# Kernel optimization log

Hardware: AMD Instinct MI355X
Metric: run time of the kernel (lower is better)

## Reference

```python
import jax, jax.numpy as jnp
import numpy as np

B = 128          # episodes
L = 512          # static pad length per episode (support or query)
LAMBDA_K_TAU = 0.1


def _masked_cov(x, mask, lengths):
    # x: [B, L, D]; mask: [B, L, 1]; lengths: [B] (float counts)
    x = x * mask
    mean = x.sum(axis=1) / lengths[:, None]                    # [B, D]
    c = (x - mean[:, None, :]) * mask                          # [B, L, D]
    cov = jnp.einsum('bld,ble->bde', c, c)                     # [B, D, D]
    return cov / (lengths - 1.0)[:, None, None]


def _calc_label_cov_inv(task_cov, label_cov):
    d = task_cov.shape[-1]
    eye = jnp.eye(d, dtype=task_cov.dtype)
    m = LAMBDA_K_TAU * label_cov + (1.0 - LAMBDA_K_TAU) * task_cov + 0.1 * eye
    return jnp.linalg.inv(m)


def _separate_qsl(graph_reprs, labels, is_query, batch_index):
    # Re-batch flat [N, D] into padded per-episode support/query tensors.
    N, D = graph_reprs.shape
    g = batch_index * 2 + is_query                             # group id
    perm = jnp.argsort(g)                                      # stable sort
    gs = g[perm]
    first = jnp.searchsorted(gs, gs, side='left')
    rank = jnp.arange(N) - first                               # index within group
    b = batch_index[perm]
    q = is_query[perm]
    row_s = jnp.where(q == 0, rank, L)                         # dummy row L for other kind
    row_q = jnp.where(q == 1, rank, L)
    xp = graph_reprs[perm]
    sup = jnp.zeros((B, L + 1, D), graph_reprs.dtype).at[b, row_s].set(xp)[:, :L]
    qry = jnp.zeros((B, L + 1, D), graph_reprs.dtype).at[b, row_q].set(xp)[:, :L]
    sup_lab = jnp.zeros((B, L + 1), labels.dtype).at[b, row_s].set(labels[perm])[:, :L]
    isq = is_query.astype(jnp.float32)
    sup_len = jnp.zeros((B,), jnp.float32).at[batch_index].add(1.0 - isq)
    qry_len = jnp.zeros((B,), jnp.float32).at[batch_index].add(isq)
    return sup, sup_lab, sup_len, qry, qry_len


def setup_inputs() -> dict:
    key = jax.random.key(0)
    k0, k1, k2, k3 = jax.random.split(key, 4)
    N, D = 49152, 512
    graph_reprs = jax.random.normal(k0, (N, D), jnp.float32)
    labels = jax.random.randint(k1, (N,), 0, 2)
    is_query = jax.random.randint(k2, (N,), 0, 2)
    batch_index = jnp.sort(jax.random.randint(k3, (N,), 0, B))
    log_scale = jnp.full((1,), np.log(1.0 / 16.0), jnp.float32)
    return {"graph_reprs": graph_reprs, "log_scale": log_scale,
            "labels": labels, "is_query": is_query, "batch_index": batch_index}


def reference(graph_reprs, log_scale, labels, is_query, batch_index):
    sup, sup_lab, sup_len, qry, qry_len = _separate_qsl(graph_reprs, labels, is_query, batch_index)
    f = jnp.float32
    support_mask = (jnp.arange(L)[None, :] < sup_len[:, None]).astype(f)[..., None]  # [B,L,1]
    mpos = (sup_lab == 1).astype(f)[..., None] * support_mask
    mneg = (sup_lab == 0).astype(f)[..., None] * support_mask

    pos_mean = (sup * mpos).sum(axis=1) / mpos.sum(axis=1)     # [B, D]
    neg_mean = (sup * mneg).sum(axis=1) / mneg.sum(axis=1)

    task_cov = _masked_cov(sup, support_mask, sup_len)
    pos_cnt = mpos.sum(axis=(1, 2))
    neg_cnt = mneg.sum(axis=(1, 2))
    # Masked covariance == cov of boolean-extracted, re-batched class subsets.
    pos_cov = _masked_cov(sup, mpos, pos_cnt)
    neg_cov = _masked_cov(sup, mneg, neg_cnt)

    pos_inv = _calc_label_cov_inv(task_cov, pos_cov)
    neg_inv = _calc_label_cov_inv(task_cov, neg_cov)

    query_mask = (jnp.arange(L)[None, :] < qry_len[:, None]).astype(f)  # [B, L]
    pos_diff = qry - pos_mean[:, None, :]
    neg_diff = qry - neg_mean[:, None, :]
    # Faithful to original einsum (sums inv over its second index):
    pos_maha = jnp.einsum('bik,bkx,bij->bi', pos_diff, pos_inv, pos_diff) * query_mask
    neg_maha = jnp.einsum('bik,bkx,bij->bi', neg_diff, neg_inv, neg_diff) * query_mask

    logits = jnp.stack([neg_maha, pos_maha], axis=-1)          # [B, L, 2]
    return logits * jnp.exp(log_scale)
```

## Files before the change

### kernel.cpp

```cpp
#include <hip/hip_runtime.h>
#include <cstdint>
#include <cstddef>

#define EPISODES 128
#define LPAD     512
#define DDIM     512
#define NS_CAP   320
#define GTILE    64
#define NPAIRS   15
#define CG_ITERS 14
#define GL_F4    9984
#define KCH      64
#define XBF_ROW  1024

typedef __attribute__((ext_vector_type(8))) __bf16 bf16x8;
typedef __attribute__((ext_vector_type(4))) float  floatx4;

__device__ __forceinline__ int lower_bound_dev(const int* __restrict__ a, int n, int key){
    int lo = 0, hi = n;
    while(lo < hi){
        int m = (lo + hi) >> 1;
        if(a[m] < key) lo = m + 1; else hi = m;
    }
    return lo;
}

__device__ __forceinline__ float4 f4add(float4 a, float4 b){
    return make_float4(a.x+b.x, a.y+b.y, a.z+b.z, a.w+b.w);
}
__device__ __forceinline__ float4 f4fma(float s, float4 a, float4 acc){
    return make_float4(acc.x + s*a.x, acc.y + s*a.y, acc.z + s*a.z, acc.w + s*a.w);
}
__device__ __forceinline__ float f4dot(float4 a, float4 b){
    return a.x*b.x + a.y*b.y + a.z*b.z + a.w*b.w;
}
__device__ __forceinline__ float f4sum(float4 a){ return (a.x+a.y)+(a.z+a.w); }

__device__ __forceinline__ unsigned short f2bf(float x){
    unsigned u = __float_as_uint(x);
    u += 0x7FFFu + ((u >> 16) & 1u);
    return (unsigned short)(u >> 16);
}
__device__ __forceinline__ float bf2f(unsigned short h){
    return __uint_as_float(((unsigned)h) << 16);
}
__device__ __forceinline__ void cvt_hilo(float4 x, ushort4& hh, ushort4& ll){
    hh.x = f2bf(x.x); ll.x = f2bf(x.x - bf2f(hh.x));
    hh.y = f2bf(x.y); ll.y = f2bf(x.y - bf2f(hh.y));
    hh.z = f2bf(x.z); ll.z = f2bf(x.z - bf2f(hh.z));
    hh.w = f2bf(x.w); ll.w = f2bf(x.w - bf2f(hh.w));
}

__device__ __forceinline__ float rdlanef(float v, int l){
    return __int_as_float(__builtin_amdgcn_readlane(__float_as_int(v), l));
}
__device__ __forceinline__ float dotb(float4 g, float4 u, int l){
    return g.x*rdlanef(u.x,l) + g.y*rdlanef(u.y,l)
         + g.z*rdlanef(u.z,l) + g.w*rdlanef(u.w,l);
}
__device__ __forceinline__ void gload_lds16(const void* g, void* l){
    __builtin_amdgcn_global_load_lds(
        (const __attribute__((address_space(1))) void*)g,
        (__attribute__((address_space(3))) void*)l,
        16, 0, 0);
}

__global__ __launch_bounds__(256) void k_prep(
        const int* __restrict__ labels, const int* __restrict__ is_query,
        const int* __restrict__ bidx, const float* __restrict__ X, int N,
        int* __restrict__ sup_idx, int* __restrict__ qry_idx,
        int* __restrict__ sup_lab, int* __restrict__ counts,
        float* __restrict__ task_mean, float* __restrict__ pos_mean,
        float* __restrict__ neg_mean, float* __restrict__ row_sums2,
        unsigned short* __restrict__ Xbf)
{
    const int bid  = blockIdx.x;
    const int b    = bid >> 1;
    const int h    = bid & 1;
    const int tid  = threadIdx.x;
    const int lane = tid & 63;
    const int wave = tid >> 6;

    __shared__ int s_start, s_end;
    __shared__ int wq[4];
    __shared__ int s_runq, s_npos;
    __shared__ int   sidx[NS_CAP];
    __shared__ float slabf[NS_CAP];
    __shared__ float4 pa[4][64];
    __shared__ float4 pp[4][64];

    if(tid == 0){
        s_start = lower_bound_dev(bidx, N, b);
        s_end   = lower_bound_dev(bidx, N, b + 1);
        s_runq  = 0;
        s_npos  = 0;
    }
    __syncthreads();
    const int start = s_start, end = s_end;

    for(int base = start; base < end; base += 256){
        int idx   = base + tid;
        bool valid = idx < end;
        int q   = valid ? is_query[idx] : 0;
        int lab = valid ? labels[idx]   : 0;
        unsigned long long m = __ballot(q == 1);
        if(lane == 0) wq[wave] = __popcll(m);
        __syncthreads();
        int woff = 0;
        for(int w = 0; w < wave; w++) woff += wq[w];
        int qbefore = __popcll(m & ((1ull << lane) - 1ull)) + woff;
        int runq0 = s_runq;
        int chunk_total = wq[0] + wq[1] + wq[2] + wq[3];
        if(valid){
            int pos_in_seg = idx - start;
            if(q){
                int qr = runq0 + qbefore;
                if(h == 0 && qr < LPAD) qry_idx[b * LPAD + qr] = idx;
            } else {
                int sr = pos_in_seg - runq0 - qbefore;
                if(sr < LPAD){
                    if(h == 0){
                        sup_idx[b * LPAD + sr] = idx;
                        sup_lab[b * LPAD + sr] = lab;
                    }
                    if(sr < NS_CAP){ sidx[sr] = idx; slabf[sr] = (float)lab; }
                    if(lab == 1) atomicAdd(&s_npos, 1);
                }
            }
        }
        __syncthreads();
        if(tid == 0) s_runq = runq0 + chunk_total;
        __syncthreads();
    }

    const int nq   = s_runq;
    const int ns   = (end - start) - nq;
    const int npos = s_npos;
    const int nneg = ns - npos;
    if(h == 0 && tid == 0){
        counts[b*4 + 0] = ns;
        counts[b*4 + 1] = nq;
        counts[b*4 + 2] = npos;
        counts[b*4 + 3] = nneg;
    }
    const int nsb = min(ns, NS_CAP);

    const float4* X4 = (const float4*)X;
    const int colg = h*64 + lane;
    float4 sa = make_float4(0.f,0.f,0.f,0.f);
    float4 sp = make_float4(0.f,0.f,0.f,0.f);
    int r = wave;
    for(; r + 12 < nsb; r += 16){
        int n0 = sidx[r], n1 = sidx[r+4], n2 = sidx[r+8], n3 = sidx[r+12];
        float l0 = slabf[r], l1 = slabf[r+4], l2 = slabf[r+8], l3 = slabf[r+12];
        float4 x0 = X4[(size_t)n0*128 + colg];
        float4 x1 = X4[(size_t)n1*128 + colg];
        float4 x2 = X4[(size_t)n2*128 + colg];
        float4 x3 = X4[(size_t)n3*128 + colg];
        sa = f4add(sa, f4add(f4add(x0,x1), f4add(x2,x3)));
        sp = f4fma(l0,x0, f4fma(l1,x1, f4fma(l2,x2, f4fma(l3,x3, sp))));
        {
            ushort4 hh, ll;
            size_t rb;
            rb = ((size_t)(b*NS_CAP + r   ) << 10);
            cvt_hilo(x0, hh, ll);
            *(ushort4*)&Xbf[rb + colg*4] = hh;  *(ushort4*)&Xbf[rb + 512 + colg*4] = ll;
            rb = ((size_t)(b*NS_CAP + r+4 ) << 10);
            cvt_hilo(x1, hh, ll);
            *(ushort4*)&Xbf[rb + colg*4] = hh;  *(ushort4*)&Xbf[rb + 512 + colg*4] = ll;
            rb = ((size_t)(b*NS_CAP + r+8 ) << 10);
            cvt_hilo(x2, hh, ll);
            *(ushort4*)&Xbf[rb + colg*4] = hh;  *(ushort4*)&Xbf[rb + 512 + colg*4] = ll;
            rb = ((size_t)(b*NS_CAP + r+12) << 10);
            cvt_hilo(x3, hh, ll);
            *(ushort4*)&Xbf[rb + colg*4] = hh;  *(ushort4*)&Xbf[rb + 512 + colg*4] = ll;
        }
        float r0s = f4sum(x0), r1s = f4sum(x1), r2s = f4sum(x2), r3s = f4sum(x3);
        #pragma unroll
        for(int off = 32; off; off >>= 1){
            r0s += __shfl_xor(r0s, off); r1s += __shfl_xor(r1s, off);
            r2s += __shfl_xor(r2s, off); r3s += __shfl_xor(r3s, off);
        }
        if(lane == 0){
            row_sums2[(b*LPAD + r   )*2 + h] = r0s;
            row_sums2[(b*LPAD + r+4 )*2 + h] = r1s;
            row_sums2[(b*LPAD + r+8 )*2 + h] = r2s;
            row_sums2[(b*LPAD + r+12)*2 + h] = r3s;
        }
    }
    for(; r < nsb; r += 4){
        int n = sidx[r];
        float l = slabf[r];
        float4 x = X4[(size_t)n*128 + colg];
        sa = f4add(sa, x);
        sp = f4fma(l, x, sp);
        {
            ushort4 hh, ll;
            size_t rb = ((size_t)(b*NS_CAP + r) << 10);
            cvt_hilo(x, hh, ll);
            *(ushort4*)&Xbf[rb + colg*4] = hh;  *(ushort4*)&Xbf[rb + 512 + colg*4] = ll;
        }
        float rs = f4sum(x);
        #pragma unroll
        for(int off = 32; off; off >>= 1) rs += __shfl_xor(rs, off);
        if(lane == 0) row_sums2[(b*LPAD + r)*2 + h] = rs;
    }
    {
        const int padf = min((nsb + 63) & ~63, NS_CAP);
        ushort4 z; z.x = z.y = z.z = z.w = 0;
        for(int rz = nsb + wave; rz < padf; rz += 4){
            size_t rb = ((size_t)(b*NS_CAP + rz) << 10);
            *(ushort4*)&Xbf[rb + colg*4] = z;
            *(ushort4*)&Xbf[rb + 512 + colg*4] = z;
        }
    }
    pa[wave][lane] = sa;
    pp[wave][lane] = sp;
    __syncthreads();
    if(tid < 64){
        float4 A = f4add(f4add(pa[0][tid],pa[1][tid]), f4add(pa[2][tid],pa[3][tid]));
        float4 P = f4add(f4add(pp[0][tid],pp[1][tid]), f4add(pp[2][tid],pp[3][tid]));
        float4 Nn = make_float4(A.x-P.x, A.y-P.y, A.z-P.z, A.w-P.w);
        float ia = 1.f/(float)ns, ip = 1.f/(float)npos, in = 1.f/(float)nneg;
        int c = b*128 + h*64 + tid;
        ((float4*)task_mean)[c] = make_float4(A.x*ia, A.y*ia, A.z*ia, A.w*ia);
        ((float4*)pos_mean )[c] = make_float4(P.x*ip, P.y*ip, P.z*ip, P.w*ip);
        ((float4*)neg_mean )[c] = make_float4(Nn.x*in, Nn.y*in, Nn.z*in, Nn.w*in);
    }
}

__global__ __launch_bounds__(256) void k_gram(
        const unsigned short* __restrict__ Xbf,
        const int* __restrict__ counts, float* __restrict__ G0)
{
    const int bid = blockIdx.x;
    const int b   = bid / NPAIRS;
    int tp = bid % NPAIRS;
    int ti = 0;
    while((ti+1)*(ti+2)/2 <= tp) ti++;
    const int tj  = tp - ti*(ti+1)/2;
    const int tid = threadIdx.x;
    const int lane = tid & 63;
    const int wave = tid >> 6;

    const int ns  = counts[b*4 + 0];
    const int nsc = min(ns, NS_CAP);
    if(ti * GTILE >= nsc) return;
    const bool diag = (ti == tj);

    __shared__ __align__(16) unsigned short SM[4 * GTILE * 64];
    unsigned short* const SAh = SM;
    unsigned short* const SAl = SM + 4096;
    const unsigned short* Bh = diag ? SAh : (SM + 8192);
    const unsigned short* Bl = diag ? SAl : (SM + 12288);

    const int r8  = lane >> 3;
    const int blk = lane & 7;
    const int fr = lane & 15;
    const int fq = (lane >> 4) * 8;
    const int ry = (wave >> 1) * 32;
    const int cx = (wave & 1) * 32;

    floatx4 acc[2][2];
    acc[0][0] = (floatx4){0.f,0.f,0.f,0.f};
    acc[0][1] = (floatx4){0.f,0.f,0.f,0.f};
    acc[1][0] = (floatx4){0.f,0.f,0.f,0.f};
    acc[1][1] = (floatx4){0.f,0.f,0.f,0.f};

    const int xr = blk ^ r8;
    for(int k0 = 0; k0 < DDIM; k0 += KCH){
        __syncthreads();
        #pragma unroll
        for(int i = 0; i < 4; i++){
            int e  = wave*4 + i;
            int pl = e >> 3, g = e & 7;
            int row = g*8 + r8;
            const unsigned short* src = Xbf
                + ((size_t)(b*NS_CAP + ti*GTILE + row) << 10)
                + pl*512 + k0 + (xr << 3);
            gload_lds16(src, SM + pl*4096 + row*64 + blk*8);
        }
        if(!diag){
            #pragma unroll
            for(int i = 0; i < 4; i++){
                int e  = wave*4 + i;
                int pl = e >> 3, g = e & 7;
                int row = g*8 + r8;
                const unsigned short* src = Xbf
                    + ((size_t)(b*NS_CAP + tj*GTILE + row) << 10)
                    + pl*512 + k0 + (xr << 3);
                gload_lds16(src, SM + 8192 + pl*4096 + row*64 + blk*8);
            }
        }
        __syncthreads();
        #pragma unroll
        for(int ks = 0; ks < KCH; ks += 32){
            const int j  = (ks + fq) >> 3;
            const int jx = (j ^ (fr & 7)) << 3;
            bf16x8 ah0 = *(const bf16x8*)&SAh[(ry      + fr)*64 + jx];
            bf16x8 ah1 = *(const bf16x8*)&SAh[(ry + 16 + fr)*64 + jx];
            bf16x8 al0 = *(const bf16x8*)&SAl[(ry      + fr)*64 + jx];
            bf16x8 al1 = *(const bf16x8*)&SAl[(ry + 16 + fr)*64 + jx];
            bf16x8 bh0 = *(const bf16x8*)&Bh [(cx      + fr)*64 + jx];
            bf16x8 bh1 = *(const bf16x8*)&Bh [(cx + 16 + fr)*64 + jx];
            bf16x8 bl0 = *(const bf16x8*)&Bl [(cx      + fr)*64 + jx];
            bf16x8 bl1 = *(const bf16x8*)&Bl [(cx + 16 + fr)*64 + jx];
            acc[0][0] = __builtin_amdgcn_mfma_f32_16x16x32_bf16(ah0, bh0, acc[0][0], 0,0,0);
            acc[0][1] = __builtin_amdgcn_mfma_f32_16x16x32_bf16(ah0, bh1, acc[0][1], 0,0,0);
            acc[1][0] = __builtin_amdgcn_mfma_f32_16x16x32_bf16(ah1, bh0, acc[1][0], 0,0,0);
            acc[1][1] = __builtin_amdgcn_mfma_f32_16x16x32_bf16(ah1, bh1, acc[1][1], 0,0,0);
            acc[0][0] = __builtin_amdgcn_mfma_f32_16x16x32_bf16(ah0, bl0, acc[0][0], 0,0,0);
            acc[0][1] = __builtin_amdgcn_mfma_f32_16x16x32_bf16(ah0, bl1, acc[0][1], 0,0,0);
            acc[1][0] = __builtin_amdgcn_mfma_f32_16x16x32_bf16(ah1, bl0, acc[1][0], 0,0,0);
            acc[1][1] = __builtin_amdgcn_mfma_f32_16x16x32_bf16(ah1, bl1, acc[1][1], 0,0,0);
            acc[0][0] = __builtin_amdgcn_mfma_f32_16x16x32_bf16(al0, bh0, acc[0][0], 0,0,0);
            acc[0][1] = __builtin_amdgcn_mfma_f32_16x16x32_bf16(al0, bh1, acc[0][1], 0,0,0);
            acc[1][0] = __builtin_amdgcn_mfma_f32_16x16x32_bf16(al1, bh0, acc[1][0], 0,0,0);
            acc[1][1] = __builtin_amdgcn_mfma_f32_16x16x32_bf16(al1, bh1, acc[1][1], 0,0,0);
        }
    }

    float4* Gf4 = (float4*)(G0 + (size_t)b * NS_CAP * NS_CAP);
    const int q = lane >> 4, j = lane & 15;
    #pragma unroll
    for(int sy = 0; sy < 2; sy++)
        #pragma unroll
        for(int sx = 0; sx < 2; sx++){
            int cq = ((ti*GTILE + ry + sy*16) >> 2) + q;
            int t  = tj*GTILE + cx + sx*16 + j;
            Gf4[(size_t)cq * NS_CAP + t] =
                make_float4(acc[sy][sx].x, acc[sy][sx].y, acc[sy][sx].z, acc[sy][sx].w);
        }

    if(!diag){
        __syncthreads();
        float* Tb = (float*)SM;
        #pragma unroll
        for(int sy = 0; sy < 2; sy++)
            #pragma unroll
            for(int sx = 0; sx < 2; sx++){
                int r0 = ry + sy*16 + 4*q;
                int c  = cx + sx*16 + j;
                Tb[(r0+0)*68 + c] = acc[sy][sx].x;
                Tb[(r0+1)*68 + c] = acc[sy][sx].y;
                Tb[(r0+2)*68 + c] = acc[sy][sx].z;
                Tb[(r0+3)*68 + c] = acc[sy][sx].w;
            }
        __syncthreads();
        for(int e = tid; e < 16*GTILE; e += 256){
            int cc = e >> 6;
            int r  = e & 63;
            float4 v = *(const float4*)&Tb[r*68 + 4*cc];
            Gf4[(size_t)(tj*16 + cc) * NS_CAP + ti*GTILE + r] = v;
        }
    }
}

extern __shared__ float4 gl4[];

__global__ __launch_bounds__(512, 2) void k_cgc(
        const float* __restrict__ X, const float* __restrict__ G0,
        const int* __restrict__ sup_idx, const int* __restrict__ sup_lab,
        const int* __restrict__ counts, const float* __restrict__ row_sums2,
        float* __restrict__ vout)
{
    const int bid  = blockIdx.x;
    const int sys  = ((bid & 7) << 5) | (bid >> 3);
    const int b    = sys >> 1;
    const int cls  = sys & 1;
    const int tid  = threadIdx.x;
    const int lane = tid & 63;
    const int wave = tid >> 6;
    const int half = tid >> 8;
    const int hrow = tid & 255;

    __shared__ __align__(16) float u[NS_CAP];
    __shared__ int   idx_l[NS_CAP];
    __shared__ float P[64];
    __shared__ float exch[256];

    const int ns   = counts[b*4 + 0];
    const int nsc  = min(ns, NS_CAP);
    const int ncls = cls ? counts[b*4 + 2] : counts[b*4 + 3];
    const float c_task = 0.9f / (float)(ns - 1);
    const float c_cls  = 0.1f / (float)(ncls - 1);
    const float inv_ns = 1.f / (float)ns;
    const float inv_nc = 1.f / (float)ncls;
    const float4* G4 = (const float4*)(G0 + (size_t)b * NS_CAP * NS_CAP);
    const float4* u4 = (const float4*)u;
    const int nf4 = (nsc + 3) >> 2;
    const int c4l = min(nf4, GL_F4 / nsc);
    const int c4m = min(nf4, ((nf4 >> 1) + 3) & ~3);

    const bool mth = tid < NS_CAP;
    const bool own = tid < nsc;
    float mfl = 0.f, sraw = 0.f;
    if(own){
        mfl  = (sup_lab[b*LPAD + tid] == cls) ? 1.f : 0.f;
        float2 rs = ((const float2*)row_sums2)[b*LPAD + tid];
        sraw = rs.x + rs.y;
    }
    for(int s = tid; s < nsc; s += 512) idx_l[s] = sup_idx[b*LPAD + s];
    if(tid < 64) P[tid] = 0.f;

    {
        const int nchunk = (nsc + 63) >> 6;
        for(int ch = 0; ch < nchunk; ch++){
            const int t = (ch << 6) + lane;
            const bool act = t < nsc;
            const float4* gsrc = G4 + t;
            float4*       ldst = gl4 + t;
            for(int c4 = wave; c4 < c4l; c4 += 8){
                if(act) gload_lds16(gsrc + (size_t)c4 * NS_CAP, ldst + c4 * nsc);
            }
        }
    }
    __syncthreads();

    auto bundle = [&](float v0, float v1, float v2, float v3, float v4,
                      float* S){
        #pragma unroll
        for(int off = 32; off; off >>= 1){
            v0 += __shfl_xor(v0, off); v1 += __shfl_xor(v1, off);
            v2 += __shfl_xor(v2, off); v3 += __shfl_xor(v3, off);
            v4 += __shfl_xor(v4, off);
        }
        if(lane == 0){
            P[wave*8 + 0] = v0; P[wave*8 + 1] = v1; P[wave*8 + 2] = v2;
            P[wave*8 + 3] = v3; P[wave*8 + 4] = v4;
        }
        __syncthreads();
        float pv = P[lane];
        pv += __shfl_xor(pv, 8);
        pv += __shfl_xor(pv, 16);
        pv += __shfl_xor(pv, 32);
        S[0] = __shfl(pv, 0); S[1] = __shfl(pv, 1); S[2] = __shfl(pv, 2);
        S[3] = __shfl(pv, 3); S[4] = __shfl(pv, 4);
    };

    const bool fastu = (nf4 <= 64);

    auto matvec = [&]() -> float {
        if(fastu){
            float p = 0.f;
            if(((wave & 3) << 6) < nsc){
                float4 ubc = u4[lane < nf4 ? lane : 0];
                asm volatile("" : "+v"(ubc.x), "+v"(ubc.y), "+v"(ubc.z), "+v"(ubc.w));
                const bool ownr = hrow < nsc;
                const int row = ownr ? hrow : (nsc - 1);
                const float4* gq = gl4 + row;
                float s0 = 0.f, s1 = 0.f, s2 = 0.f, s3 = 0.f;
                const int lo = half ? c4m : 0;
                const int hi = half ? nf4 : c4m;
                const int lim = min(hi, c4l);
                int c4 = lo;
                for(; c4 + 8 <= lim; c4 += 8){
                    float4 g0 = gq[(c4+0)*nsc], g1 = gq[(c4+1)*nsc];
                    float4 g2 = gq[(c4+2)*nsc], g3 = gq[(c4+3)*nsc];
                    float4 g4_ = gq[(c4+4)*nsc], g5 = gq[(c4+5)*nsc];
                    float4 g6 = gq[(c4+6)*nsc], g7 = gq[(c4+7)*nsc];
                    s0 += dotb(g0, ubc, c4+0); s1 += dotb(g1, ubc, c4+1);
                    s2 += dotb(g2, ubc, c4+2); s3 += dotb(g3, ubc, c4+3);
                    s0 += dotb(g4_, ubc, c4+4); s1 += dotb(g5, ubc, c4+5);
                    s2 += dotb(g6, ubc, c4+6); s3 += dotb(g7, ubc, c4+7);
                }
                for(; c4 < lim; c4++) s0 += dotb(gq[c4*nsc], ubc, c4);
                for(; c4 + 4 <= hi; c4 += 4){
                    float4 h0 = G4[(size_t)(c4+0)*NS_CAP + row];
                    float4 h1 = G4[(size_t)(c4+1)*NS_CAP + row];
                    float4 h2 = G4[(size_t)(c4+2)*NS_CAP + row];
                    float4 h3 = G4[(size_t)(c4+3)*NS_CAP + row];
                    s0 += dotb(h0, ubc, c4+0); s1 += dotb(h1, ubc, c4+1);
                    s2 += dotb(h2, ubc, c4+2); s3 += dotb(h3, ubc, c4+3);
                }
                for(; c4 < hi; c4++)
                    s0 += dotb(G4[(size_t)c4*NS_CAP + row], ubc, c4);
                p = ownr ? ((s0 + s1) + (s2 + s3)) : 0.f;
            }
            if(half) exch[hrow] = p;
            __syncthreads();
            float t = (half == 0 && own) ? (p + exch[hrow]) : 0.f;
            return t;
        } else {
            float s0 = 0.f, s1 = 0.f, s2 = 0.f, s3 = 0.f;
            if(own){
                const float4* gq = gl4 + tid;
                int c4 = 0;
                for(; c4 + 8 <= c4l; c4 += 8){
                    float4 g0 = gq[(c4+0)*nsc], g1 = gq[(c4+1)*nsc];
                    float4 g2 = gq[(c4+2)*nsc], g3 = gq[(c4+3)*nsc];
                    float4 g4_ = gq[(c4+4)*nsc], g5 = gq[(c4+5)*nsc];
                    float4 g6 = gq[(c4+6)*nsc], g7 = gq[(c4+7)*nsc];
                    s0 += f4dot(g0, u4[c4+0]); s1 += f4dot(g1, u4[c4+1]);
                    s2 += f4dot(g2, u4[c4+2]); s3 += f4dot(g3, u4[c4+3]);
                    s0 += f4dot(g4_, u4[c4+4]); s1 += f4dot(g5, u4[c4+5]);
                    s2 += f4dot(g6, u4[c4+6]); s3 += f4dot(g7, u4[c4+7]);
                }
                for(; c4 < c4l; c4++) s0 += f4dot(gq[c4*nsc], u4[c4]);
                for(; c4 + 8 <= nf4; c4 += 8){
                    float4 g[8];
                    #pragma unroll
                    for(int jj = 0; jj < 8; jj++) g[jj] = G4[(size_t)(c4+jj)*NS_CAP + tid];
                    #pragma unroll
                    for(int jj = 0; jj < 8; jj++){
                        float d = f4dot(g[jj], u4[c4+jj]);
                        if((jj & 3) == 0) s0 += d; else if((jj & 3) == 1) s1 += d;
                        else if((jj & 3) == 2) s2 += d; else s3 += d;
                    }
                }
                for(; c4 < nf4; c4++) s0 += f4dot(G4[(size_t)c4*NS_CAP + tid], u4[c4]);
            }
            float t = (s0 + s1) + (s2 + s3);
            return own ? t : 0.f;
        }
    };

    float S[5];
    bundle(sraw, mfl * sraw, 0.f, 0.f, 0.f, S);
    float A0 = S[0] * inv_ns, A1 = S[1] * inv_nc;
    float cr = own ? -10.f * (c_task*(sraw - A0) + mfl*c_cls*(sraw - A1)) : 0.f;
    if(mth) u[tid] = cr;
    __syncthreads();
    float tr = matvec();

    float cp = 0.f, cq = 0.f, tq = 0.f, cx = 0.f;
    float gamma_old = 1.f, alpha_old = 1.f;
    bool first = true;

    for(int it = 0; it < CG_ITERS; ++it){
        bundle(tr, mfl*tr, tr*tr, mfl*tr*tr, tr*cr, S);
        A0 = S[0] * inv_ns; A1 = S[1] * inv_nc;
        float gamma = S[4];
        float delta = 0.1f*gamma + c_task*(S[2] - S[0]*A0)
                                 + c_cls *(S[3] - S[1]*A1);
        float beta  = first ? 0.f : gamma / gamma_old;
        float denom = first ? delta : (delta - beta * gamma / alpha_old);
        float alpha = (gamma < 1e-30f) ? 0.f : gamma / denom;
        float ur = own ? (c_task*(tr - A0) + mfl*c_cls*(tr - A1)) : 0.f;
        float cw = 0.1f*cr + ur;
        cp = cr + beta * cp;
        cq = cw + beta * cq;
        cx += alpha * cp;
        if(it == CG_ITERS - 1 || gamma < 1e-26f) break;
        if(mth) u[tid] = ur;
        __syncthreads();
        float gv = matvec();
        float tw = 0.1f*tr + gv;
        tq = tw + beta * tq;
        cr -= alpha * cq;
        tr -= alpha * tq;
        gamma_old = gamma; alpha_old = alpha; first = false;
    }

    __syncthreads();
    if(mth) u[tid] = own ? cx : 0.f;
    __syncthreads();
    const float4* X4 = (const float4*)X;
    const int f4c = tid & 127;
    const int rg  = tid >> 7;
    float4 acc = make_float4(0.f,0.f,0.f,0.f);
    int s = rg;
    for(; s + 28 < nsc; s += 32){
        int n0 = idx_l[s],    n1 = idx_l[s+4],  n2 = idx_l[s+8],  n3 = idx_l[s+12];
        int n4 = idx_l[s+16], n5 = idx_l[s+20], n6 = idx_l[s+24], n7 = idx_l[s+28];
        float w0 = u[s],    w1 = u[s+4],  w2 = u[s+8],  w3 = u[s+12];
        float w4 = u[s+16], w5 = u[s+20], w6 = u[s+24], w7 = u[s+28];
        float4 x0 = X4[(size_t)n0*128 + f4c];
        float4 x1 = X4[(size_t)n1*128 + f4c];
        float4 x2 = X4[(size_t)n2*128 + f4c];
        float4 x3 = X4[(size_t)n3*128 + f4c];
        float4 x4 = X4[(size_t)n4*128 + f4c];
        float4 x5 = X4[(size_t)n5*128 + f4c];
        float4 x6 = X4[(size_t)n6*128 + f4c];
        float4 x7 = X4[(size_t)n7*128 + f4c];
        acc = f4fma(w0,x0, f4fma(w1,x1, f4fma(w2,x2, f4fma(w3,x3, acc))));
        acc = f4fma(w4,x4, f4fma(w5,x5, f4fma(w6,x6, f4fma(w7,x7, acc))));
    }
    for(; s < nsc; s += 4)
        acc = f4fma(u[s], X4[(size_t)idx_l[s]*128 + f4c], acc);
    gl4[rg*128 + f4c] = acc;
    __syncthreads();
    if(tid < 128){
        float4 v = f4add(f4add(gl4[tid], gl4[128+tid]),
                         f4add(gl4[256+tid], gl4[384+tid]));
        v.x += 10.f; v.y += 10.f; v.z += 10.f; v.w += 10.f;
        ((float4*)vout)[(size_t)sys * 128 + tid] = v;
    }
}

__global__ __launch_bounds__(256) void k_out(
        const float* __restrict__ X,
        const int* __restrict__ qry_idx, const int* __restrict__ counts,
        const float* __restrict__ pos_mean, const float* __restrict__ neg_mean,
        const float* __restrict__ vsol, const float* __restrict__ log_scale,
        float* __restrict__ out)
{
    const int bid  = blockIdx.x;
    const int b    = bid >> 1;
    const int h    = bid & 1;
    const int tid  = threadIdx.x;
    const int lane = tid & 63;
    const int wave = tid >> 6;

    __shared__ __align__(16) float vpos[DDIM];
    __shared__ __align__(16) float vneg[DDIM];
    __shared__ float red4[4][4];
    __shared__ float sc[4];

    const int nq  = counts[b*4 + 1];
    const int nqc = min(nq, LPAD);
    const float scale = expf(log_scale[0]);

    float pm0 = pos_mean[b*DDIM + tid], pm1 = pos_mean[b*DDIM + tid + 256];
    float nm0 = neg_mean[b*DDIM + tid], nm1 = neg_mean[b*DDIM + tid + 256];
    float vp0 = vsol[(size_t)(b*2 + 1) * DDIM + tid];
    float vp1 = vsol[(size_t)(b*2 + 1) * DDIM + tid + 256];
    float vn0 = vsol[(size_t)(b*2 + 0) * DDIM + tid];
    float vn1 = vsol[(size_t)(b*2 + 0) * DDIM + tid + 256];
    vpos[tid] = vp0; vpos[tid + 256] = vp1;
    vneg[tid] = vn0; vneg[tid + 256] = vn1;

    float smp = pm0 + pm1;
    float smn = nm0 + nm1;
    float mvp = pm0 * vp0 + pm1 * vp1;
    float mvn = nm0 * vn0 + nm1 * vn1;
    #pragma unroll
    for(int off = 32; off; off >>= 1){
        smp += __shfl_xor(smp, off);
        smn += __shfl_xor(smn, off);
        mvp += __shfl_xor(mvp, off);
        mvn += __shfl_xor(mvn, off);
    }
    if(lane == 0){
        red4[wave][0] = smp; red4[wave][1] = smn;
        red4[wave][2] = mvp; red4[wave][3] = mvn;
    }
    __syncthreads();
    if(tid < 4) sc[tid] = red4[0][tid] + red4[1][tid] + red4[2][tid] + red4[3][tid];
    __syncthreads();

    const float4* vp4 = (const float4*)vpos;
    const float4* vn4 = (const float4*)vneg;
    const float4 vpa = vp4[lane], vpb = vp4[lane + 64];
    const float4 vna = vn4[lane], vnb = vn4[lane + 64];
    for(int r = wave + 4*h; r < nqc; r += 16){
        int r2 = r + 8;
        bool has2 = r2 < nqc;
        int n  = qry_idx[b * LPAD + r];
        int n2 = qry_idx[b * LPAD + (has2 ? r2 : r)];
        const float4* xr = (const float4*)(X + (size_t)n  * DDIM);
        const float4* yr = (const float4*)(X + (size_t)n2 * DDIM);
        float4 x0 = xr[lane], x1 = xr[lane + 64];
        float4 y0 = yr[lane], y1 = yr[lane + 64];
        float tp = f4dot(x0, vpa) + f4dot(x1, vpb);
        float tn = f4dot(x0, vna) + f4dot(x1, vnb);
        float sx = f4sum(x0) + f4sum(x1);
        float tp2 = f4dot(y0, vpa) + f4dot(y1, vpb);
        float tn2 = f4dot(y0, vna) + f4dot(y1, vnb);
        float sx2 = f4sum(y0) + f4sum(y1);
        #pragma unroll
        for(int off = 32; off; off >>= 1){
            tp  += __shfl_xor(tp,  off);
            tn  += __shfl_xor(tn,  off);
            sx  += __shfl_xor(sx,  off);
            tp2 += __shfl_xor(tp2, off);
            tn2 += __shfl_xor(tn2, off);
            sx2 += __shfl_xor(sx2, off);
        }
        if(lane == 0){
            float mp = (tp - sc[2]) * (sx - sc[0]);
            float mn = (tn - sc[3]) * (sx - sc[1]);
            ((float2*)out)[(size_t)b * LPAD + r] = make_float2(mn * scale, mp * scale);
            if(has2){
                float mp2 = (tp2 - sc[2]) * (sx2 - sc[0]);
                float mn2 = (tn2 - sc[3]) * (sx2 - sc[1]);
                ((float2*)out)[(size_t)b * LPAD + r2] = make_float2(mn2 * scale, mp2 * scale);
            }
        }
    }
    const int lo = max(nqc, h * 256), hi = (h + 1) * 256;
    for(int r = lo + tid; r < hi; r += 256)
        ((float2*)out)[(size_t)b * LPAD + r] = make_float2(0.f, 0.f);
}

extern "C" void kernel_launch(void* const* d_in, const int* in_sizes, int n_in,
                              void* d_out, int out_size, void* d_ws, size_t ws_size,
                              hipStream_t stream)
{
    const float* X         = (const float*)d_in[0];
    const float* log_scale = (const float*)d_in[1];
    const int*   labels    = (const int*)d_in[2];
    const int*   is_query  = (const int*)d_in[3];
    const int*   bidx      = (const int*)d_in[4];
    const int N = in_sizes[2];

    char* ws = (char*)d_ws;
    auto alloc = [&](size_t bytes) -> char* {
        char* p = ws;
        ws += (bytes + 255) & ~(size_t)255;
        return p;
    };
    int*   sup_idx   = (int*)  alloc((size_t)EPISODES * LPAD * sizeof(int));
    int*   qry_idx   = (int*)  alloc((size_t)EPISODES * LPAD * sizeof(int));
    int*   sup_lab   = (int*)  alloc((size_t)EPISODES * LPAD * sizeof(int));
    int*   counts    = (int*)  alloc((size_t)EPISODES * 4 * sizeof(int));
    float* task_mean = (float*)alloc((size_t)EPISODES * DDIM * sizeof(float));
    float* pos_mean  = (float*)alloc((size_t)EPISODES * DDIM * sizeof(float));
    float* neg_mean  = (float*)alloc((size_t)EPISODES * DDIM * sizeof(float));
    float* vsol      = (float*)alloc((size_t)EPISODES * 2 * DDIM * sizeof(float));
    float* row_sums2 = (float*)alloc((size_t)EPISODES * LPAD * 2 * sizeof(float));
    float* G0        = (float*)alloc((size_t)EPISODES * NS_CAP * NS_CAP * sizeof(float));
    unsigned short* Xbf = (unsigned short*)alloc(
                          (size_t)EPISODES * NS_CAP * XBF_ROW * sizeof(unsigned short));
    (void)ws_size;
    (void)task_mean;

    k_prep<<<EPISODES*2, 256, 0, stream>>>(labels, is_query, bidx, X, N,
                                           sup_idx, qry_idx, sup_lab, counts,
                                           task_mean, pos_mean, neg_mean, row_sums2,
                                           Xbf);
    k_gram<<<EPISODES * NPAIRS, 256, 0, stream>>>(Xbf, counts, G0);
    k_cgc<<<EPISODES * 2, 512, GL_F4 * sizeof(float4), stream>>>(
                                            X, G0, sup_idx, sup_lab, counts,
                                            row_sums2, vsol);
    k_out<<<EPISODES*2, 256, 0, stream>>>(X, qry_idx, counts, pos_mean, neg_mean,
                                          vsol, log_scale, (float*)d_out);
}
```

Measured before the change: 297.1 us.

## Keep Gram matrix rows in registers for CG matvec instead of shared memory

The CG solver's matvec now holds the first 48 float4 columns of each thread's Gram row in registers, loaded once before the iterations. Only any remaining columns are staged in LDS, which shrinks the shared-memory staging size. The split-half matvec with its exchange buffer and extra barrier is removed, so each thread owns one full row. The launch bound drops the two-blocks-per-CU hint to make room for the 192 extra VGPRs, which risks lower occupancy or register spills.

```diff
diff --git a/kernel.cpp b/kernel.cpp
--- a/kernel.cpp
+++ b/kernel.cpp
@@ -9,9 +9,10 @@
 #define GTILE    64
 #define NPAIRS   15
 #define CG_ITERS 14
-#define GL_F4    9984
+#define GL_F4    4096
 #define KCH      64
 #define XBF_ROW  1024
+#define GREG     48
 
 typedef __attribute__((ext_vector_type(8))) __bf16 bf16x8;
 typedef __attribute__((ext_vector_type(4))) float  floatx4;
@@ -358,7 +359,7 @@
 
 extern __shared__ float4 gl4[];
 
-__global__ __launch_bounds__(512, 2) void k_cgc(
+__global__ __launch_bounds__(512) void k_cgc(
         const float* __restrict__ X, const float* __restrict__ G0,
         const int* __restrict__ sup_idx, const int* __restrict__ sup_lab,
         const int* __restrict__ counts, const float* __restrict__ row_sums2,
@@ -371,13 +372,10 @@
     const int tid  = threadIdx.x;
     const int lane = tid & 63;
     const int wave = tid >> 6;
-    const int half = tid >> 8;
-    const int hrow = tid & 255;
 
     __shared__ __align__(16) float u[NS_CAP];
     __shared__ int   idx_l[NS_CAP];
     __shared__ float P[64];
-    __shared__ float exch[256];
 
     const int ns   = counts[b*4 + 0];
     const int nsc  = min(ns, NS_CAP);
@@ -389,8 +387,6 @@
     const float4* G4 = (const float4*)(G0 + (size_t)b * NS_CAP * NS_CAP);
     const float4* u4 = (const float4*)u;
     const int nf4 = (nsc + 3) >> 2;
-    const int c4l = min(nf4, GL_F4 / nsc);
-    const int c4m = min(nf4, ((nf4 >> 1) + 3) & ~3);
 
     const bool mth = tid < NS_CAP;
     const bool own = tid < nsc;
@@ -403,15 +399,30 @@
     for(int s = tid; s < nsc; s += 512) idx_l[s] = sup_idx[b*LPAD + s];
     if(tid < 64) P[tid] = 0.f;
 
-    {
+    const bool fastu   = (nf4 <= 64);
+    const bool haverow = ((wave << 6) < nsc);
+
+    float4 g[GREG];
+    if(fastu && haverow){
+        #pragma unroll
+        for(int c4 = 0; c4 < GREG; c4++){
+            float4 v = G4[(size_t)c4 * NS_CAP + tid];
+            bool live = (4*c4 < nsc);
+            g[c4].x = live ? v.x : 0.f;
+            g[c4].y = live ? v.y : 0.f;
+            g[c4].z = live ? v.z : 0.f;
+            g[c4].w = live ? v.w : 0.f;
+        }
+    }
+
+    if(fastu && nf4 > GREG){
         const int nchunk = (nsc + 63) >> 6;
         for(int ch = 0; ch < nchunk; ch++){
             const int t = (ch << 6) + lane;
             const bool act = t < nsc;
-            const float4* gsrc = G4 + t;
-            float4*       ldst = gl4 + t;
-            for(int c4 = wave; c4 < c4l; c4 += 8){
-                if(act) gload_lds16(gsrc + (size_t)c4 * NS_CAP, ldst + c4 * nsc);
+            for(int c4 = GREG + wave; c4 < nf4; c4 += 8){
+                if(act) gload_lds16(G4 + (size_t)c4 * NS_CAP + t,
+                                    gl4 + (c4 - GREG) * nsc + t);
             }
         }
     }
@@ -438,80 +449,44 @@
         S[3] = __shfl(pv, 3); S[4] = __shfl(pv, 4);
     };
 
-    const bool fastu = (nf4 <= 64);
-
     auto matvec = [&]() -> float {
+        float t = 0.f;
         if(fastu){
-            float p = 0.f;
-            if(((wave & 3) << 6) < nsc){
+            if(haverow){
                 float4 ubc = u4[lane < nf4 ? lane : 0];
                 asm volatile("" : "+v"(ubc.x), "+v"(ubc.y), "+v"(ubc.z), "+v"(ubc.w));
-                const bool ownr = hrow < nsc;
-                const int row = ownr ? hrow : (nsc - 1);
-                const float4* gq = gl4 + row;
                 float s0 = 0.f, s1 = 0.f, s2 = 0.f, s3 = 0.f;
-                const int lo = half ? c4m : 0;
-                const int hi = half ? nf4 : c4m;
-                const int lim = min(hi, c4l);
-                int c4 = lo;
-                for(; c4 + 8 <= lim; c4 += 8){
-                    float4 g0 = gq[(c4+0)*nsc], g1 = gq[(c4+1)*nsc];
-                    float4 g2 = gq[(c4+2)*nsc], g3 = gq[(c4+3)*nsc];
-                    float4 g4_ = gq[(c4+4)*nsc], g5 = gq[(c4+5)*nsc];
-                    float4 g6 = gq[(c4+6)*nsc], g7 = gq[(c4+7)*nsc];
-                    s0 += dotb(g0, ubc, c4+0); s1 += dotb(g1, ubc, c4+1);
-                    s2 += dotb(g2, ubc, c4+2); s3 += dotb(g3, ubc, c4+3);
-                    s0 += dotb(g4_, ubc, c4+4); s1 += dotb(g5, ubc, c4+5);
-                    s2 += dotb(g6, ubc, c4+6); s3 += dotb(g7, ubc, c4+7);
+                #pragma unroll
+                for(int c4 = 0; c4 < GREG; c4 += 4){
+                    s0 += dotb(g[c4+0], ubc, c4+0);
+                    s1 += dotb(g[c4+1], ubc, c4+1);
+                    s2 += dotb(g[c4+2], ubc, c4+2);
+                    s3 += dotb(g[c4+3], ubc, c4+3);
                 }
-                for(; c4 < lim; c4++) s0 += dotb(gq[c4*nsc], ubc, c4);
-                for(; c4 + 4 <= hi; c4 += 4){
-                    float4 h0 = G4[(size_t)(c4+0)*NS_CAP + row];
-                    float4 h1 = G4[(size_t)(c4+1)*NS_CAP + row];
-                    float4 h2 = G4[(size_t)(c4+2)*NS_CAP + row];
-                    float4 h3 = G4[(size_t)(c4+3)*NS_CAP + row];
-                    s0 += dotb(h0, ubc, c4+0); s1 += dotb(h1, ubc, c4+1);
-                    s2 += dotb(h2, ubc, c4+2); s3 += dotb(h3, ubc, c4+3);
+                if(nf4 > GREG){
+                    const int row = own ? tid : (nsc - 1);
+                    for(int c4 = GREG; c4 < nf4; c4++)
+                        s0 += f4dot(gl4[(c4 - GREG)*nsc + row], u4[c4]);
                 }
-                for(; c4 < hi; c4++)
-                    s0 += dotb(G4[(size_t)c4*NS_CAP + row], ubc, c4);
-                p = ownr ? ((s0 + s1) + (s2 + s3)) : 0.f;
+                t = (s0 + s1) + (s2 + s3);
             }
-            if(half) exch[hrow] = p;
-            __syncthreads();
-            float t = (half == 0 && own) ? (p + exch[hrow]) : 0.f;
-            return t;
+            return own ? t : 0.f;
         } else {
             float s0 = 0.f, s1 = 0.f, s2 = 0.f, s3 = 0.f;
             if(own){
-                const float4* gq = gl4 + tid;
                 int c4 = 0;
-                for(; c4 + 8 <= c4l; c4 += 8){
-                    float4 g0 = gq[(c4+0)*nsc], g1 = gq[(c4+1)*nsc];
-                    float4 g2 = gq[(c4+2)*nsc], g3 = gq[(c4+3)*nsc];
-                    float4 g4_ = gq[(c4+4)*nsc], g5 = gq[(c4+5)*nsc];
-                    float4 g6 = gq[(c4+6)*nsc], g7 = gq[(c4+7)*nsc];
-                    s0 += f4dot(g0, u4[c4+0]); s1 += f4dot(g1, u4[c4+1]);
-                    s2 += f4dot(g2, u4[c4+2]); s3 += f4dot(g3, u4[c4+3]);
-                    s0 += f4dot(g4_, u4[c4+4]); s1 += f4dot(g5, u4[c4+5]);
-                    s2 += f4dot(g6, u4[c4+6]); s3 += f4dot(g7, u4[c4+7]);
-                }
-                for(; c4 < c4l; c4++) s0 += f4dot(gq[c4*nsc], u4[c4]);
-                for(; c4 + 8 <= nf4; c4 += 8){
-                    float4 g[8];
-                    #pragma unroll
-                    for(int jj = 0; jj < 8; jj++) g[jj] = G4[(size_t)(c4+jj)*NS_CAP + tid];
-                    #pragma unroll
-                    for(int jj = 0; jj < 8; jj++){
-                        float d = f4dot(g[jj], u4[c4+jj]);
-                        if((jj & 3) == 0) s0 += d; else if((jj & 3) == 1) s1 += d;
-                        else if((jj & 3) == 2) s2 += d; else s3 += d;
-                    }
+                for(; c4 + 4 <= nf4; c4 += 4){
+                    float4 h0 = G4[(size_t)(c4+0)*NS_CAP + tid];
+                    float4 h1 = G4[(size_t)(c4+1)*NS_CAP + tid];
+                    float4 h2 = G4[(size_t)(c4+2)*NS_CAP + tid];
+                    float4 h3 = G4[(size_t)(c4+3)*NS_CAP + tid];
+                    s0 += f4dot(h0, u4[c4+0]); s1 += f4dot(h1, u4[c4+1]);
+                    s2 += f4dot(h2, u4[c4+2]); s3 += f4dot(h3, u4[c4+3]);
                 }
                 for(; c4 < nf4; c4++) s0 += f4dot(G4[(size_t)c4*NS_CAP + tid], u4[c4]);
             }
-            float t = (s0 + s1) + (s2 + s3);
-            return own ? t : 0.f;
+            float tt = (s0 + s1) + (s2 + s3);
+            return own ? tt : 0.f;
         }
     };
 
```

Result: faster. 287.9 us (-3.1%).
